# Performance work log

Measured on AMD Instinct MI355X. Metric: run time of the kernel, lower is better.

## Reference

```python
import jax, jax.numpy as jnp
import numpy as np

N_E = 8192
E_DIM = 256
BETA = 0.25


def setup_inputs() -> dict:
    key = jax.random.key(0)
    k1, k2 = jax.random.split(key)
    z = jax.random.normal(k1, (4, 256, 16, 16, 16), dtype=jnp.float32)
    weight = jax.random.normal(k2, (N_E, E_DIM), dtype=jnp.float32)
    return {"z": z, "weight": weight}


def reference(z, weight):
    # b c l h w -> b l h w c
    zc = jnp.transpose(z, (0, 2, 3, 4, 1))
    zf = zc.reshape(-1, E_DIM)  # [N, D]
    n = zf.shape[0]

    # squared euclidean distances to all codes: [N, n_e]
    d = (jnp.sum(zf * zf, axis=1, keepdims=True)
         + jnp.sum(weight * weight, axis=1)
         - 2.0 * jnp.einsum('bd,nd->bn', zf, weight))
    idx = jnp.argmin(d, axis=1)  # [N] int

    z_q = weight[idx].reshape(zc.shape)  # codebook gather

    # histogram of code usage (equivalent to one-hot mean, without the NxK one-hot)
    counts = jnp.zeros((N_E,), dtype=zf.dtype).at[idx].add(1.0)
    avg_probs = counts / jnp.asarray(n, zf.dtype)
    perplexity = jnp.exp(-jnp.sum(avg_probs * jnp.log(avg_probs + 1e-10)))
    unique = jnp.sum(counts > 0).astype(jnp.int32)

    # commitment loss (z_q detached) + straight-through estimator
    loss = BETA * jnp.mean((jax.lax.stop_gradient(z_q) - zc) ** 2)
    z_q_st = zc + jax.lax.stop_gradient(z_q - zc)

    # b l h w c -> b c l h w
    z_q_out = jnp.transpose(z_q_st, (0, 4, 1, 2, 3))
    return z_q_out, loss, perplexity, unique, idx
```

## Files before the change

kernel.cpp:

```cpp
#include <hip/hip_runtime.h>

#define NQ     16384
#define EDIM   256
#define NE     8192
#define LHW    4096
#define BETA   0.25f

#define WS_WSQ    0
#define WS_CNT    32768
#define WS_LOSS   65536
#define WS_IDX    65792
#define WS_BEST   131328
#define WS_APACK  2359552
#define WS_BPACK  10748160
#define WS_NEED   14942464

typedef __attribute__((ext_vector_type(8))) short bf16x8;
typedef __attribute__((ext_vector_type(4))) float f32x4;

__device__ __forceinline__ unsigned f32_sortable(float f) {
    unsigned b = __float_as_uint(f);
    return b ^ ((unsigned)((int)b >> 31) | 0x80000000u);
}
__device__ __forceinline__ unsigned short bf16_rn(float f) {
    unsigned u = __float_as_uint(f);
    return (unsigned short)((u + 0x7FFFu + ((u >> 16) & 1u)) >> 16);
}

__global__ __launch_bounds__(1024) void pack_all(const float* __restrict__ w,
                                                 const float* __restrict__ z,
                                                 float* __restrict__ wsq,
                                                 unsigned* __restrict__ Bp32,
                                                 unsigned* __restrict__ Ap32,
                                                 unsigned* __restrict__ counts,
                                                 float* __restrict__ loss,
                                                 unsigned* __restrict__ done) {
    __shared__ unsigned lds[64 * 129];
    int tid = threadIdx.x;
    if (blockIdx.x < 512) {
        int wave = tid >> 6, lane = tid & 63;
        int row = blockIdx.x * 16 + wave;
        if (blockIdx.x < 8) {
            counts[blockIdx.x * 1024 + tid] = 0u;
            if (blockIdx.x == 0 && tid == 0) { loss[0] = 0.f; done[0] = 0u; }
        }
        float4 v = *(const float4*)(w + (size_t)row * EDIM + lane * 4);
        double s = (double)v.x * v.x + (double)v.y * v.y +
                   (double)v.z * v.z + (double)v.w * v.w;
        unsigned p0 = (unsigned)bf16_rn(v.x) | ((unsigned)bf16_rn(v.y) << 16);
        unsigned p1 = (unsigned)bf16_rn(v.z) | ((unsigned)bf16_rn(v.w) << 16);
        *(uint2*)(Bp32 + (size_t)row * 128 + lane * 2) = make_uint2(p0, p1);
        #pragma unroll
        for (int off = 32; off; off >>= 1) s += __shfl_xor(s, off, 64);
        if (lane == 0) wsq[row] = (float)s;
    } else {
        int bz = blockIdx.x - 512;
        int tn = tid & 63, tc = tid >> 6;
        int n0 = bz * 64;
        int n = n0 + tn;
        int b = n >> 12, lhw = n & 4095;
        #pragma unroll
        for (int cc = 0; cc < 16; cc += 2) {
            int d = tc * 16 + cc;
            float v0 = z[((size_t)b * EDIM + d) * LHW + lhw];
            float v1 = z[((size_t)b * EDIM + d + 1) * LHW + lhw];
            lds[tn * 129 + (d >> 1)] =
                (unsigned)bf16_rn(v0) | ((unsigned)bf16_rn(v1) << 16);
        }
        __syncthreads();
        #pragma unroll
        for (int p = 0; p < 8; ++p) {
            int flat = p * 1024 + tid;
            int row = flat >> 7, c = flat & 127;
            Ap32[(size_t)(n0 + row) * 128 + c] = lds[row * 129 + c];
        }
    }
}

__global__ __launch_bounds__(256) void wsq_kernel(const float* __restrict__ w,
                                                  float* __restrict__ wsq) {
    int wave = threadIdx.x >> 6, lane = threadIdx.x & 63;
    int row = blockIdx.x * 4 + wave;
    float4 v = *(const float4*)(w + (size_t)row * EDIM + lane * 4);
    double s = (double)v.x * v.x + (double)v.y * v.y +
               (double)v.z * v.z + (double)v.w * v.w;
    #pragma unroll
    for (int off = 32; off; off >>= 1) s += __shfl_xor(s, off, 64);
    if (lane == 0) wsq[row] = (float)s;
}

__global__ __launch_bounds__(256, 3) void dist_mfma(const unsigned short* __restrict__ Ap,
                                                    const unsigned short* __restrict__ Bp,
                                                    const float* __restrict__ wsq,
                                                    unsigned* __restrict__ s1) {
    __shared__ __align__(16) unsigned short lds_b[2][128 * 64];
    int tid = threadIdx.x, lane = tid & 63, w = tid >> 6;
    int x = blockIdx.x, nt = blockIdx.y;
    int quad = lane >> 4, col = lane & 15;
    int rsel = lane >> 3, seg = lane & 7;

    const unsigned short* arow = Ap + (size_t)(nt * 128 + w * 32 + col) * 256;
    const unsigned short* Bbase = Bp + (size_t)(x * 128) * 256;

    f32x4 acc[2][8];
    #pragma unroll
    for (int i = 0; i < 2; ++i)
        #pragma unroll
        for (int j = 0; j < 8; ++j) acc[i][j] = (f32x4){0.f, 0.f, 0.f, 0.f};

    auto stage_chunk = [&](int kc, int bsel) {
        int k0s = kc * 64;
        #pragma unroll
        for (int p = 0; p < 4; ++p) {
            int c = w * 4 + p;
            const unsigned short* gb =
                Bbase + (size_t)(c * 8 + rsel) * 256 + k0s + ((seg ^ (rsel & 7)) * 8);
            __builtin_amdgcn_global_load_lds(
                (const __attribute__((address_space(1))) void*)gb,
                (__attribute__((address_space(3))) void*)(&lds_b[bsel][c * 512]),
                16, 0, 0);
        }
    };

    stage_chunk(0, 0);

    #pragma unroll
    for (int kcc = 0; kcc < 4; ++kcc) {
        int k0 = kcc * 64;
        int cur = kcc & 1;
        bf16x8 af[2][2];
        #pragma unroll
        for (int i = 0; i < 2; ++i)
            #pragma unroll
            for (int h = 0; h < 2; ++h)
                af[i][h] = *(const bf16x8*)(arow + i * 16 * 256 + k0 + h * 32 + quad * 8);
        asm volatile("" ::: "memory");
        if (kcc < 3) {
            stage_chunk(kcc + 1, cur ^ 1);
            asm volatile("s_waitcnt vmcnt(8)" ::: "memory");
        } else {
            asm volatile("s_waitcnt vmcnt(4)" ::: "memory");
        }
        __builtin_amdgcn_s_barrier();
        asm volatile("" ::: "memory");
        __builtin_amdgcn_s_setprio(1);
        #pragma unroll
        for (int h = 0; h < 2; ++h) {
            bf16x8 bf[8];
            #pragma unroll
            for (int j = 0; j < 8; ++j)
                bf[j] = *(const bf16x8*)(&lds_b[cur][(j * 16 + col) * 64 +
                                         (((h * 4 + quad) ^ (col & 7)) * 8)]);
            #pragma unroll
            for (int i = 0; i < 2; ++i)
                #pragma unroll
                for (int j = 0; j < 8; ++j)
                    acc[i][j] = __builtin_amdgcn_mfma_f32_16x16x32_bf16(
                        af[i][h], bf[j], acc[i][j], 0, 0, 0);
        }
        __builtin_amdgcn_s_setprio(0);
        asm volatile("" ::: "memory");
        if (kcc < 3) {
            __builtin_amdgcn_s_barrier();
            asm volatile("" ::: "memory");
        }
    }

    unsigned m1[2][4], m2[2][4];
    #pragma unroll
    for (int i = 0; i < 2; ++i)
        #pragma unroll
        for (int r = 0; r < 4; ++r) { m1[i][r] = 0xFFFFFFFFu; m2[i][r] = 0xFFFFFFFFu; }
    #pragma unroll
    for (int j = 0; j < 8; ++j) {
        int e = x * 128 + j * 16 + col;
        unsigned jc = (unsigned)(j * 16 + col);
        float wq_off = wsq[e] + 4096.0f;
        #pragma unroll
        for (int i = 0; i < 2; ++i)
            #pragma unroll
            for (int r = 0; r < 4; ++r) {
                float d = fmaf(-2.0f, acc[i][j][r], wq_off);
                unsigned k = (__float_as_uint(d) & 0xFFFFFF80u) | jc;
                unsigned mx = (m1[i][r] > k) ? m1[i][r] : k;
                m1[i][r] = (m1[i][r] < k) ? m1[i][r] : k;
                m2[i][r] = (m2[i][r] < mx) ? m2[i][r] : mx;
            }
    }
    #pragma unroll
    for (int i = 0; i < 2; ++i)
        #pragma unroll
        for (int r = 0; r < 4; ++r) {
            unsigned a1 = m1[i][r], a2 = m2[i][r];
            #pragma unroll
            for (int off = 1; off < 16; off <<= 1) {
                unsigned b1 = __shfl_xor(a1, off, 64);
                unsigned b2 = __shfl_xor(a2, off, 64);
                unsigned lo1 = a1 < b1 ? a1 : b1;
                unsigned hi1 = a1 < b1 ? b1 : a1;
                unsigned lo2 = a2 < b2 ? a2 : b2;
                a1 = lo1;
                a2 = hi1 < lo2 ? hi1 : lo2;
            }
            if (col == 0) {
                int q = nt * 128 + w * 32 + i * 16 + quad * 4 + r;
                size_t o = (size_t)q * 128 + x * 2;
                s1[o] = a1; s1[o + 1] = a2;
            }
        }
}

__global__ __launch_bounds__(256) void refine_kernel(const float* __restrict__ z,
                                                     const float* __restrict__ w,
                                                     const float* __restrict__ wsq,
                                                     const unsigned* __restrict__ s1,
                                                     unsigned* __restrict__ idxarr) {
    __shared__ float lds_z[4][260];
    int tid = threadIdx.x, lane = tid & 63, wv = tid >> 6;
    int q0 = blockIdx.x * 4;
    int q = q0 + wv;
    int b = q0 >> 12, lhw0 = q0 & 4095;
    {
        float4 zc = *(const float4*)(z + ((size_t)b * EDIM + tid) * LHW + lhw0);
        lds_z[0][tid] = zc.x; lds_z[1][tid] = zc.y;
        lds_z[2][tid] = zc.z; lds_z[3][tid] = zc.w;
    }
    uint2 kk2 = *(const uint2*)(s1 + (size_t)q * 128 + lane * 2);
    unsigned long long a1 =
        ((unsigned long long)(kk2.x >> 7) << 13) | (unsigned)(lane * 128 + (kk2.x & 127u));
    unsigned long long a2 =
        ((unsigned long long)(kk2.y >> 7) << 13) | (unsigned)(lane * 128 + (kk2.y & 127u));
    #pragma unroll
    for (int off = 1; off < 8; off <<= 1) {
        unsigned long long b1 = __shfl_xor(a1, off, 64);
        unsigned long long b2 = __shfl_xor(a2, off, 64);
        unsigned long long lo1 = a1 < b1 ? a1 : b1;
        unsigned long long hi1 = a1 < b1 ? b1 : a1;
        unsigned long long lo2 = a2 < b2 ? a2 : b2;
        a1 = lo1;
        a2 = hi1 < lo2 ? hi1 : lo2;
    }
    __syncthreads();
    float zv[4];
    #pragma unroll
    for (int t = 0; t < 4; ++t)
        zv[t] = lds_z[wv][lane * 4 + t];
    unsigned long long bestk = ~0ull;
    #pragma unroll
    for (int c = 0; c < 16; ++c) {
        int src = (c >> 1) * 8;
        unsigned long long kc = (c & 1) ? __shfl(a2, src, 64) : __shfl(a1, src, 64);
        unsigned e = (unsigned)(kc & (unsigned long long)(NE - 1));
        float4 wv4 = *(const float4*)(w + (size_t)e * EDIM + lane * 4);
        float p = zv[0] * wv4.x + zv[1] * wv4.y + zv[2] * wv4.z + zv[3] * wv4.w;
        #pragma unroll
        for (int off = 32; off; off >>= 1) p += __shfl_xor(p, off, 64);
        float d = wsq[e] - 2.0f * p;
        unsigned long long key = ((unsigned long long)f32_sortable(d) << 32) | e;
        if (key < bestk) bestk = key;
    }
    if (lane == 0) idxarr[q] = (unsigned)(bestk & 0xFFFFFFFFull);
}

__global__ __launch_bounds__(256, 2) void dist_fp32(const float* __restrict__ z,
                                                    const float* __restrict__ w,
                                                    const float* __restrict__ wsq,
                                                    unsigned long long* __restrict__ best) {
    __shared__ float lds_a[32 * 128];
    __shared__ float lds_b[32 * 132];
    int tid = threadIdx.x;
    int tx = tid & 15, ty = tid >> 4;
    int n0 = blockIdx.y * 128;
    int bb_ = n0 >> 12, lhw0 = n0 & 4095;
    const float* zb = z + (size_t)bb_ * (EDIM * LHW) + lhw0;
    int ebase = blockIdx.x * 2048;
    unsigned long long runmin[8];
    #pragma unroll
    for (int i = 0; i < 8; ++i) runmin[i] = ~0ull;
    float acc[64];
    for (int et = 0; et < 16; ++et) {
        int e0 = ebase + et * 128;
        #pragma unroll
        for (int i = 0; i < 64; ++i) acc[i] = 0.f;
        for (int kc = 0; kc < 8; ++kc) {
            int k0 = kc * 32;
            #pragma unroll
            for (int p = 0; p < 4; ++p) {
                int f = p * 256 + tid;
                int kk = f >> 5, nn4 = f & 31;
                float4 v = *(const float4*)(zb + (size_t)(k0 + kk) * LHW + nn4 * 4);
                *((float4*)(lds_a + kk * 128 + nn4 * 4)) = v;
            }
            #pragma unroll
            for (int p = 0; p < 4; ++p) {
                int f = p * 256 + tid;
                int ee = f >> 3, kk4 = f & 7;
                float4 v = *(const float4*)(w + (size_t)(e0 + ee) * EDIM + k0 + kk4 * 4);
                lds_b[(kk4 * 4 + 0) * 132 + ee] = v.x;
                lds_b[(kk4 * 4 + 1) * 132 + ee] = v.y;
                lds_b[(kk4 * 4 + 2) * 132 + ee] = v.z;
                lds_b[(kk4 * 4 + 3) * 132 + ee] = v.w;
            }
            __syncthreads();
            #pragma unroll
            for (int k = 0; k < 32; ++k) {
                float a[8], bv[8];
                *(float4*)(a)      = *(float4*)(lds_a + k * 128 + ty * 8);
                *(float4*)(a + 4)  = *(float4*)(lds_a + k * 128 + ty * 8 + 4);
                *(float4*)(bv)     = *(float4*)(lds_b + k * 132 + tx * 8);
                *(float4*)(bv + 4) = *(float4*)(lds_b + k * 132 + tx * 8 + 4);
                #pragma unroll
                for (int i = 0; i < 8; ++i)
                    #pragma unroll
                    for (int j = 0; j < 8; ++j)
                        acc[i * 8 + j] = fmaf(a[i], bv[j], acc[i * 8 + j]);
            }
            __syncthreads();
        }
        #pragma unroll
        for (int i = 0; i < 8; ++i) {
            unsigned long long m = runmin[i];
            #pragma unroll
            for (int j = 0; j < 8; ++j) {
                int e = e0 + tx * 8 + j;
                float d = wsq[e] - 2.0f * acc[i * 8 + j];
                unsigned long long key =
                    ((unsigned long long)f32_sortable(d) << 32) | (unsigned)e;
                m = (m < key) ? m : key;
            }
            runmin[i] = m;
        }
    }
    #pragma unroll
    for (int i = 0; i < 8; ++i) {
        unsigned long long kk = runmin[i];
        #pragma unroll
        for (int off = 8; off >= 1; off >>= 1) {
            unsigned long long o = __shfl_xor(kk, off, 16);
            kk = (kk < o) ? kk : o;
        }
        if (tx == 0) atomicMin(&best[n0 + ty * 8 + i], kk);
    }
}

__global__ __launch_bounds__(256) void extract_idx(const unsigned long long* __restrict__ best,
                                                   unsigned* __restrict__ idxarr) {
    int n = blockIdx.x * 256 + threadIdx.x;
    idxarr[n] = (unsigned)(best[n] & 0xFFFFFFFFull) & (NE - 1);
}

__global__ __launch_bounds__(1024) void gather_kernel(const float* __restrict__ z,
                                                      const float* __restrict__ w,
                                                      const unsigned* __restrict__ idxarr,
                                                      unsigned* __restrict__ counts,
                                                      float* __restrict__ loss,
                                                      unsigned* __restrict__ done,
                                                      float* __restrict__ out,
                                                      float* __restrict__ out_idx,
                                                      float* __restrict__ out_scalars) {
    __shared__ int idx_s[64];
    __shared__ float wl[64 * 257];
    __shared__ float lsum[16];
    __shared__ int usum[16];
    __shared__ unsigned lastflag;
    int tid = threadIdx.x;
    int n0 = blockIdx.x * 64;
    if (tid < 64) {
        int idx = (int)(idxarr[n0 + tid] & (NE - 1));
        idx_s[tid] = idx;
        out_idx[n0 + tid] = (float)idx;
        atomicAdd(&counts[idx], 1u);
    }
    __syncthreads();
    {
        int r0 = tid >> 8, cl = tid & 255;
        #pragma unroll
        for (int i = 0; i < 16; ++i)
            wl[(r0 + i * 4) * 257 + cl] = w[(size_t)idx_s[r0 + i * 4] * EDIM + cl];
    }
    __syncthreads();
    int tn = tid & 63, tc = tid >> 6;
    int bb_ = n0 >> 12, lhw0 = n0 & 4095;
    size_t zb = (size_t)bb_ * (EDIM * LHW) + lhw0 + tn;
    float accl = 0.f;
    #pragma unroll
    for (int cc = 0; cc < 16; ++cc) {
        int c = tc * 16 + cc;
        float wv = wl[tn * 257 + c];
        size_t a = zb + (size_t)c * LHW;
        float zv = z[a];
        float diff = wv - zv;
        out[a] = zv + diff;
        accl += diff * diff;
    }
    #pragma unroll
    for (int off = 32; off; off >>= 1) accl += __shfl_xor(accl, off, 64);
    if ((tid & 63) == 0) lsum[tid >> 6] = accl;
    __syncthreads();
    if (tid < 16) {
        float v = lsum[tid];
        v += __shfl_xor(v, 8, 16);
        v += __shfl_xor(v, 4, 16);
        v += __shfl_xor(v, 2, 16);
        v += __shfl_xor(v, 1, 16);
        if (tid == 0) atomicAdd(loss, v);
    }
    __syncthreads();
    if (tid == 0) {
        __threadfence();
        lastflag = (atomicAdd(done, 1u) == (unsigned)(NQ / 64 - 1));
    }
    __syncthreads();
    if (lastflag) {
        __threadfence();
        float s = 0.f;
        int uniq = 0;
        for (int i = tid; i < NE; i += 1024) {
            unsigned c = counts[i];
            if (c > 0) {
                float p = (float)c * (1.0f / (float)NQ);
                s += p * logf(p + 1e-10f);
                uniq++;
            }
        }
        #pragma unroll
        for (int off = 32; off; off >>= 1) {
            s += __shfl_xor(s, off, 64);
            uniq += __shfl_xor(uniq, off, 64);
        }
        if ((tid & 63) == 0) { lsum[tid >> 6] = s; usum[tid >> 6] = uniq; }
        __syncthreads();
        if (tid == 0) {
            float st = 0.f;
            int ut = 0;
            #pragma unroll
            for (int i = 0; i < 16; ++i) { st += lsum[i]; ut += usum[i]; }
            out_scalars[0] = BETA * loss[0] * (1.0f / (float)(NQ * EDIM));
            out_scalars[1] = expf(-st);
            out_scalars[2] = (float)ut;
        }
    }
}

extern "C" void kernel_launch(void* const* d_in, const int* in_sizes, int n_in,
                              void* d_out, int out_size, void* d_ws, size_t ws_size,
                              hipStream_t stream) {
    const float* z = (const float*)d_in[0];
    const float* w = (const float*)d_in[1];
    float* out = (float*)d_out;
    char* ws = (char*)d_ws;
    float* wsq = (float*)(ws + WS_WSQ);
    unsigned* counts = (unsigned*)(ws + WS_CNT);
    float* loss = (float*)(ws + WS_LOSS);
    unsigned* done = (unsigned*)(ws + WS_LOSS + 4);
    unsigned* idxarr = (unsigned*)(ws + WS_IDX);
    unsigned long long* best = (unsigned long long*)(ws + WS_BEST);
    unsigned* Ap = (unsigned*)(ws + WS_APACK);
    unsigned* Bp = (unsigned*)(ws + WS_BPACK);

    int idx_off = out_size - NQ;
    int scal_off = idx_off - 3;
    float* out_idx = out + idx_off;
    float* out_scalars = out + scal_off;

    unsigned* s1 = (unsigned*)out;

    if (ws_size >= (size_t)WS_NEED) {
        pack_all<<<768, 1024, 0, stream>>>(w, z, wsq, Bp, Ap, counts, loss, done);
        dist_mfma<<<dim3(64, 128), 256, 0, stream>>>((const unsigned short*)Ap,
                                                     (const unsigned short*)Bp, wsq, s1);
        refine_kernel<<<NQ / 4, 256, 0, stream>>>(z, w, wsq, s1, idxarr);
    } else {
        hipMemsetAsync(counts, 0, NE * sizeof(unsigned), stream);
        hipMemsetAsync(loss, 0, 8, stream);
        wsq_kernel<<<NE / 4, 256, 0, stream>>>(w, wsq);
        hipMemsetAsync(best, 0xFF, NQ * sizeof(unsigned long long), stream);
        dist_fp32<<<dim3(4, 128), 256, 0, stream>>>(z, w, wsq, best);
        extract_idx<<<NQ / 256, 256, 0, stream>>>(best, idxarr);
    }

    gather_kernel<<<NQ / 64, 1024, 0, stream>>>(z, w, idxarr, counts, loss, done,
                                                out, out_idx, out_scalars);
}
```

Baseline: 238.9 us.

## Fuse candidate refinement into gather kernel and stage z tile in LDS

Removes the separate refine_kernel and performs the fp32 top-candidate rescoring inside gather_kernel. Each block transposes its 64-query z tile into shared memory once and reuses it for both refinement and the output/loss pass. The stage-1 candidate buffer moves from the output array into workspace with a column-major (slot-major) layout, which makes the per-lane reads coalesced. This saves one launch and one global read of z. In exchange, gather blocks use more LDS, which lowers occupancy, and the refinement step gets less parallelism per block.

Result: faster. 220.2 us, median of 2 (-7.8%).

```diff
diff --git a/kernel.cpp b/kernel.cpp
--- a/kernel.cpp
+++ b/kernel.cpp
@@ -13,7 +13,8 @@
 #define WS_BEST   131328
 #define WS_APACK  2359552
 #define WS_BPACK  10748160
-#define WS_NEED   14942464
+#define WS_S1     14942464
+#define WS_NEED   23331072
 
 typedef __attribute__((ext_vector_type(8))) short bf16x8;
 typedef __attribute__((ext_vector_type(4))) float f32x4;
@@ -204,62 +205,10 @@
             }
             if (col == 0) {
                 int q = nt * 128 + w * 32 + i * 16 + quad * 4 + r;
-                size_t o = (size_t)q * 128 + x * 2;
+                size_t o = (size_t)x * (NQ * 2) + (size_t)q * 2;
                 s1[o] = a1; s1[o + 1] = a2;
             }
         }
-}
-
-__global__ __launch_bounds__(256) void refine_kernel(const float* __restrict__ z,
-                                                     const float* __restrict__ w,
-                                                     const float* __restrict__ wsq,
-                                                     const unsigned* __restrict__ s1,
-                                                     unsigned* __restrict__ idxarr) {
-    __shared__ float lds_z[4][260];
-    int tid = threadIdx.x, lane = tid & 63, wv = tid >> 6;
-    int q0 = blockIdx.x * 4;
-    int q = q0 + wv;
-    int b = q0 >> 12, lhw0 = q0 & 4095;
-    {
-        float4 zc = *(const float4*)(z + ((size_t)b * EDIM + tid) * LHW + lhw0);
-        lds_z[0][tid] = zc.x; lds_z[1][tid] = zc.y;
-        lds_z[2][tid] = zc.z; lds_z[3][tid] = zc.w;
-    }
-    uint2 kk2 = *(const uint2*)(s1 + (size_t)q * 128 + lane * 2);
-    unsigned long long a1 =
-        ((unsigned long long)(kk2.x >> 7) << 13) | (unsigned)(lane * 128 + (kk2.x & 127u));
-    unsigned long long a2 =
-        ((unsigned long long)(kk2.y >> 7) << 13) | (unsigned)(lane * 128 + (kk2.y & 127u));
-    #pragma unroll
-    for (int off = 1; off < 8; off <<= 1) {
-        unsigned long long b1 = __shfl_xor(a1, off, 64);
-        unsigned long long b2 = __shfl_xor(a2, off, 64);
-        unsigned long long lo1 = a1 < b1 ? a1 : b1;
-        unsigned long long hi1 = a1 < b1 ? b1 : a1;
-        unsigned long long lo2 = a2 < b2 ? a2 : b2;
-        a1 = lo1;
-        a2 = hi1 < lo2 ? hi1 : lo2;
-    }
-    __syncthreads();
-    float zv[4];
-    #pragma unroll
-    for (int t = 0; t < 4; ++t)
-        zv[t] = lds_z[wv][lane * 4 + t];
-    unsigned long long bestk = ~0ull;
-    #pragma unroll
-    for (int c = 0; c < 16; ++c) {
-        int src = (c >> 1) * 8;
-        unsigned long long kc = (c & 1) ? __shfl(a2, src, 64) : __shfl(a1, src, 64);
-        unsigned e = (unsigned)(kc & (unsigned long long)(NE - 1));
-        float4 wv4 = *(const float4*)(w + (size_t)e * EDIM + lane * 4);
-        float p = zv[0] * wv4.x + zv[1] * wv4.y + zv[2] * wv4.z + zv[3] * wv4.w;
-        #pragma unroll
-        for (int off = 32; off; off >>= 1) p += __shfl_xor(p, off, 64);
-        float d = wsq[e] - 2.0f * p;
-        unsigned long long key = ((unsigned long long)f32_sortable(d) << 32) | e;
-        if (key < bestk) bestk = key;
-    }
-    if (lane == 0) idxarr[q] = (unsigned)(bestk & 0xFFFFFFFFull);
 }
 
 __global__ __launch_bounds__(256, 2) void dist_fp32(const float* __restrict__ z,
@@ -351,6 +300,8 @@
 
 __global__ __launch_bounds__(1024) void gather_kernel(const float* __restrict__ z,
                                                       const float* __restrict__ w,
+                                                      const float* __restrict__ wsq,
+                                                      const unsigned* __restrict__ s1,
                                                       const unsigned* __restrict__ idxarr,
                                                       unsigned* __restrict__ counts,
                                                       float* __restrict__ loss,
@@ -358,20 +309,82 @@
                                                       float* __restrict__ out,
                                                       float* __restrict__ out_idx,
                                                       float* __restrict__ out_scalars) {
+    __shared__ float zt[64 * 272];
+    __shared__ float wl[64 * 257];
     __shared__ int idx_s[64];
-    __shared__ float wl[64 * 257];
     __shared__ float lsum[16];
     __shared__ int usum[16];
     __shared__ unsigned lastflag;
-    int tid = threadIdx.x;
+    int tid = threadIdx.x, lane = tid & 63, wv = tid >> 6;
     int n0 = blockIdx.x * 64;
-    if (tid < 64) {
-        int idx = (int)(idxarr[n0 + tid] & (NE - 1));
-        idx_s[tid] = idx;
-        out_idx[n0 + tid] = (float)idx;
-        atomicAdd(&counts[idx], 1u);
-    }
-    __syncthreads();
+    int bb_ = n0 >> 12, lhw0 = n0 & 4095;
+    const float* zb = z + (size_t)bb_ * (EDIM * LHW) + lhw0;
+
+    {
+        int l = tid & 63, dg = tid >> 6;
+        #pragma unroll
+        for (int i = 0; i < 16; ++i) {
+            int d = dg * 16 + i;
+            zt[l * 272 + d] = zb[(size_t)d * LHW + l];
+        }
+    }
+    __syncthreads();
+
+    if (s1 != nullptr) {
+        #pragma unroll
+        for (int jq = 0; jq < 4; ++jq) {
+            int ql = wv * 4 + jq;
+            int q = n0 + ql;
+            uint2 kk2 = *(const uint2*)(s1 + ((size_t)lane * NQ + q) * 2);
+            unsigned long long a1 = ((unsigned long long)(kk2.x >> 7) << 13)
+                                  | (unsigned)(lane * 128 + (kk2.x & 127u));
+            unsigned long long a2 = ((unsigned long long)(kk2.y >> 7) << 13)
+                                  | (unsigned)(lane * 128 + (kk2.y & 127u));
+            #pragma unroll
+            for (int off = 1; off < 8; off <<= 1) {
+                unsigned long long b1 = __shfl_xor(a1, off, 64);
+                unsigned long long b2 = __shfl_xor(a2, off, 64);
+                unsigned long long lo1 = a1 < b1 ? a1 : b1;
+                unsigned long long hi1 = a1 < b1 ? b1 : a1;
+                unsigned long long lo2 = a2 < b2 ? a2 : b2;
+                a1 = lo1;
+                a2 = hi1 < lo2 ? hi1 : lo2;
+            }
+            float4 zv4 = *(const float4*)(&zt[ql * 272 + lane * 4]);
+            unsigned long long bestk = ~0ull;
+            #pragma unroll
+            for (int c = 0; c < 16; ++c) {
+                int src = (c >> 1) * 8;
+                unsigned long long kc = (c & 1) ? __shfl(a2, src, 64)
+                                                : __shfl(a1, src, 64);
+                unsigned e = (unsigned)(kc & (unsigned long long)(NE - 1));
+                float4 wv4 = *(const float4*)(w + (size_t)e * EDIM + lane * 4);
+                float p = zv4.x * wv4.x + zv4.y * wv4.y +
+                          zv4.z * wv4.z + zv4.w * wv4.w;
+                #pragma unroll
+                for (int off = 32; off; off >>= 1) p += __shfl_xor(p, off, 64);
+                float d = wsq[e] - 2.0f * p;
+                unsigned long long key =
+                    ((unsigned long long)f32_sortable(d) << 32) | e;
+                if (key < bestk) bestk = key;
+            }
+            if (lane == 0) {
+                int idx = (int)(bestk & 0xFFFFFFFFull) & (NE - 1);
+                idx_s[ql] = idx;
+                out_idx[q] = (float)idx;
+                atomicAdd(&counts[idx], 1u);
+            }
+        }
+    } else {
+        if (tid < 64) {
+            int idx = (int)(idxarr[n0 + tid] & (NE - 1));
+            idx_s[tid] = idx;
+            out_idx[n0 + tid] = (float)idx;
+            atomicAdd(&counts[idx], 1u);
+        }
+    }
+    __syncthreads();
+
     {
         int r0 = tid >> 8, cl = tid & 255;
         #pragma unroll
@@ -379,23 +392,22 @@
             wl[(r0 + i * 4) * 257 + cl] = w[(size_t)idx_s[r0 + i * 4] * EDIM + cl];
     }
     __syncthreads();
+
     int tn = tid & 63, tc = tid >> 6;
-    int bb_ = n0 >> 12, lhw0 = n0 & 4095;
-    size_t zb = (size_t)bb_ * (EDIM * LHW) + lhw0 + tn;
+    size_t ob = (size_t)bb_ * (EDIM * LHW) + lhw0 + tn;
     float accl = 0.f;
     #pragma unroll
     for (int cc = 0; cc < 16; ++cc) {
         int c = tc * 16 + cc;
-        float wv = wl[tn * 257 + c];
-        size_t a = zb + (size_t)c * LHW;
-        float zv = z[a];
-        float diff = wv - zv;
-        out[a] = zv + diff;
+        float wv_ = wl[tn * 257 + c];
+        float zv = zt[tn * 272 + c];
+        float diff = wv_ - zv;
+        out[ob + (size_t)c * LHW] = zv + diff;
         accl += diff * diff;
     }
     #pragma unroll
     for (int off = 32; off; off >>= 1) accl += __shfl_xor(accl, off, 64);
-    if ((tid & 63) == 0) lsum[tid >> 6] = accl;
+    if (lane == 0) lsum[wv] = accl;
     __syncthreads();
     if (tid < 16) {
         float v = lsum[tid];
@@ -405,6 +417,7 @@
         v += __shfl_xor(v, 1, 16);
         if (tid == 0) atomicAdd(loss, v);
     }
+
     __syncthreads();
     if (tid == 0) {
         __threadfence();
@@ -428,7 +441,7 @@
             s += __shfl_xor(s, off, 64);
             uniq += __shfl_xor(uniq, off, 64);
         }
-        if ((tid & 63) == 0) { lsum[tid >> 6] = s; usum[tid >> 6] = uniq; }
+        if (lane == 0) { lsum[wv] = s; usum[wv] = uniq; }
         __syncthreads();
         if (tid == 0) {
             float st = 0.f;
@@ -457,19 +470,19 @@
     unsigned long long* best = (unsigned long long*)(ws + WS_BEST);
     unsigned* Ap = (unsigned*)(ws + WS_APACK);
     unsigned* Bp = (unsigned*)(ws + WS_BPACK);
+    unsigned* s1 = (unsigned*)(ws + WS_S1);
 
     int idx_off = out_size - NQ;
     int scal_off = idx_off - 3;
     float* out_idx = out + idx_off;
     float* out_scalars = out + scal_off;
 
-    unsigned* s1 = (unsigned*)out;
-
     if (ws_size >= (size_t)WS_NEED) {
         pack_all<<<768, 1024, 0, stream>>>(w, z, wsq, Bp, Ap, counts, loss, done);
         dist_mfma<<<dim3(64, 128), 256, 0, stream>>>((const unsigned short*)Ap,
                                                      (const unsigned short*)Bp, wsq, s1);
-        refine_kernel<<<NQ / 4, 256, 0, stream>>>(z, w, wsq, s1, idxarr);
+        gather_kernel<<<NQ / 64, 1024, 0, stream>>>(z, w, wsq, s1, idxarr, counts,
+                                                    loss, done, out, out_idx, out_scalars);
     } else {
         hipMemsetAsync(counts, 0, NE * sizeof(unsigned), stream);
         hipMemsetAsync(loss, 0, 8, stream);
@@ -477,8 +490,7 @@
         hipMemsetAsync(best, 0xFF, NQ * sizeof(unsigned long long), stream);
         dist_fp32<<<dim3(4, 128), 256, 0, stream>>>(z, w, wsq, best);
         extract_idx<<<NQ / 256, 256, 0, stream>>>(best, idxarr);
-    }
-
-    gather_kernel<<<NQ / 64, 1024, 0, stream>>>(z, w, idxarr, counts, loss, done,
-                                                out, out_idx, out_scalars);
-}
+        gather_kernel<<<NQ / 64, 1024, 0, stream>>>(z, w, wsq, nullptr, idxarr, counts,
+                                                    loss, done, out, out_idx, out_scalars);
+    }
+}
```
